# Kernel tuning notes

Hardware: AMD Instinct MI355X
Metric: run time of the kernel (lower is better)

Reference implementation:

```python
import jax, jax.numpy as jnp
import numpy as np

B, S, D, H = 2, 2048, 1024, 16
DH = D // H


def setup_inputs() -> dict:
    key = jax.random.key(0)
    ks = jax.random.split(key, 5)
    scale = 0.02
    return {
        "X": jax.random.normal(ks[0], (B, S, D), jnp.float32),
        "Wq": jax.random.normal(ks[1], (H, D, DH), jnp.float32) * scale,
        "Wk": jax.random.normal(ks[2], (H, D, DH), jnp.float32) * scale,
        "Wv": jax.random.normal(ks[3], (H, D, DH), jnp.float32) * scale,
        "Wo": jax.random.normal(ks[4], (D, D), jnp.float32) * scale,
        "bo": jnp.zeros((D,), jnp.float32),
    }


def reference(X, Wq, Wk, Wv, Wo, bo):
    # Per-head projections, batched over heads: [B,H,S,DH]
    Q = jnp.einsum('bsd,hde->bhse', X, Wq)
    K = jnp.einsum('bsd,hde->bhse', X, Wk)
    V = jnp.einsum('bsd,hde->bhse', X, Wv)
    # Scores scaled by sqrt(d_model) exactly as in the source (not sqrt(d_head))
    A = jnp.einsum('bhse,bhte->bhst', Q, K) / jnp.sqrt(jnp.float32(D))
    A = jax.nn.softmax(A, axis=-1)  # no mask in the source
    O = jnp.einsum('bhst,bhte->bhse', A, V)  # [B,H,S,DH]
    # Concat heads -> [B,S,D], then output projection
    O = jnp.transpose(O, (0, 2, 1, 3)).reshape(B, S, D)
    return O @ Wo + bo
```

## Files before the change

kernel.cpp:

```cpp
#include <hip/hip_runtime.h>
#include <math.h>

static constexpr int Bc  = 2;
static constexpr int Sc  = 2048;
static constexpr int Dc  = 1024;
static constexpr int Hc  = 16;
static constexpr int DHc = 64;

typedef short bf16x8 __attribute__((ext_vector_type(8)));
typedef float f32x4  __attribute__((ext_vector_type(4)));

static constexpr float LOG2E = 1.4426950408889634f;

static __device__ __forceinline__ unsigned short f2bf(float x) {
  union { float f; unsigned u; } v; v.f = x;
  unsigned r = v.u + 0x7FFFu + ((v.u >> 16) & 1u);
  return (unsigned short)(r >> 16);
}
static __device__ __forceinline__ float bf2f(unsigned short u) {
  union { unsigned u; float f; } v; v.u = ((unsigned)u) << 16;
  return v.f;
}
static __device__ __forceinline__ unsigned pk2bf_trunc(float a, float b) {
  return __builtin_amdgcn_perm(__float_as_uint(b), __float_as_uint(a), 0x07060302u);
}
#if __has_builtin(__builtin_amdgcn_exp2f)
#define EXP2F(x) __builtin_amdgcn_exp2f(x)
#else
#define EXP2F(x) exp2f(x)
#endif

static __device__ __forceinline__ void gload16(const void* g, void* l) {
  __builtin_amdgcn_global_load_lds(
      (const __attribute__((address_space(1))) void*)g,
      (__attribute__((address_space(3))) void*)l, 16, 0, 0);
}

__global__ __launch_bounds__(256) void prep(
    const float* __restrict__ Wq, const float* __restrict__ Wk,
    const float* __restrict__ Wv, const float* __restrict__ Wo,
    const float* __restrict__ X,
    unsigned short* __restrict__ Wt3, unsigned short* __restrict__ Wot,
    unsigned short* __restrict__ Xb) {
  const int z = blockIdx.z;
  if (z == 4) {
    size_t base = ((size_t)blockIdx.y * 16 + blockIdx.x) * 4096;
#pragma unroll
    for (int it = 0; it < 16; ++it) {
      size_t i = base + it * 256 + threadIdx.x;
      float4 v = ((const float4*)X)[i];
      ushort4 u; u.x = f2bf(v.x); u.y = f2bf(v.y); u.z = f2bf(v.z); u.w = f2bf(v.w);
      ((ushort4*)Xb)[i] = u;
    }
    return;
  }
  __shared__ unsigned short T[64][68];
  const float* src; unsigned short* dst;
  int srcld, dstld, r0, c0;
  if (z < 3) {
    const float* W = (z == 0) ? Wq : (z == 1) ? Wk : Wv;
    unsigned short* Wt = Wt3 + (size_t)z * Dc * Dc;
    int h = blockIdx.y;
    src = W + (size_t)h * Dc * DHc;  srcld = DHc; r0 = blockIdx.x * 64; c0 = 0;
    dst = Wt + (size_t)h * DHc * Dc; dstld = Dc;
  } else {
    src = Wo;  srcld = Dc; r0 = blockIdx.x * 64; c0 = blockIdx.y * 64;
    dst = Wot; dstld = Dc;
  }
#pragma unroll
  for (int it = 0; it < 16; ++it) {
    int idx = it * 256 + threadIdx.x;
    int r = idx >> 6, c = idx & 63;
    T[c][r] = f2bf(src[(size_t)(r0 + r) * srcld + c0 + c]);
  }
  __syncthreads();
#pragma unroll
  for (int it = 0; it < 4; ++it) {
    int idx = it * 256 + threadIdx.x;
    int c = idx >> 4, r4 = (idx & 15) * 4;
    ushort4 u = *(const ushort4*)&T[c][r4];
    *(ushort4*)&dst[(size_t)(c0 + c) * dstld + r0 + r4] = u;
  }
}

__global__ __launch_bounds__(512, 2) void qkv_gemm(
    const unsigned short* __restrict__ Xb, const unsigned short* __restrict__ Wt3,
    unsigned short* __restrict__ Qb, unsigned short* __restrict__ Kb,
    unsigned short* __restrict__ Vtb) {
  __shared__ alignas(16) unsigned char smem[135168];
  unsigned short (*S)[64] = (unsigned short(*)[64])smem;

  const int tid = threadIdx.x;
  const int wv = tid >> 6, lane = tid & 63;
  const int ln = lane & 15, qd = (lane >> 4) & 3;
  const int wm = wv >> 2, wn = wv & 3;
  const int lr = lane >> 3;
  const int gcol = ((lane & 7) ^ lr) * 8;
  const int paq = ln & 7;

  const int bid = blockIdx.x;
  const int l = (bid & 7) * 24 + (bid >> 3);
  const int xb = l & 15, y = l >> 4;
  const int m0 = xb * 256, n0 = y * 256;
  const int which = y >> 2;
  const int b = m0 >> 11, s0 = m0 & 2047;
  const int h0 = (y & 3) * 4;

  const unsigned short* Ap = Xb + (size_t)m0 * 1024;
  const unsigned short* Bp = Wt3 + (size_t)n0 * 1024;
  const int grow = wv * 16 + lr;

#define STG(gb, srow) do {                                                  \
    gload16((gb) + (size_t)grow * 1024 + gcol,       &S[(srow) + wv * 16][0]); \
    gload16((gb) + (size_t)(grow + 8) * 1024 + gcol, &S[(srow) + wv * 16 + 8][0]); \
  } while (0)

#define RD_A(mh, rowbase) do {                                              \
    _Pragma("unroll") for (int mt = 0; mt < 4; ++mt)                        \
      _Pragma("unroll") for (int ks = 0; ks < 2; ++ks)                      \
        af[mt][ks] = *(const bf16x8*)&S[(rowbase) + (mh) * 64 + mt * 16 + ln] \
                                       [((ks * 4 + qd) ^ paq) * 8];         \
  } while (0)

#define RD_B(nh, rowbase) do {                                              \
    _Pragma("unroll") for (int nt = 0; nt < 2; ++nt)                        \
      _Pragma("unroll") for (int ks = 0; ks < 2; ++ks)                      \
        bf[(nh) * 2 + nt][ks] = *(const bf16x8*)&S[(rowbase) + (nh) * 32 + nt * 16 + ln] \
                                                  [((ks * 4 + qd) ^ paq) * 8]; \
  } while (0)

#define MM(mh, nh) do {                                                     \
    _Pragma("unroll") for (int ks = 0; ks < 2; ++ks)                        \
      _Pragma("unroll") for (int mt = 0; mt < 4; ++mt)                      \
        _Pragma("unroll") for (int nt = 0; nt < 2; ++nt)                    \
          acc[(mh) * 4 + mt][(nh) * 2 + nt] =                               \
              __builtin_amdgcn_mfma_f32_16x16x32_bf16(                      \
                  af[mt][ks], bf[(nh) * 2 + nt][ks],                        \
                  acc[(mh) * 4 + mt][(nh) * 2 + nt], 0, 0, 0);              \
  } while (0)

#define BAR __builtin_amdgcn_s_barrier()
#define WAITL asm volatile("s_waitcnt lgkmcnt(0)" ::: "memory")
#define WAITV(n) asm volatile("s_waitcnt vmcnt(" #n ")" ::: "memory")
#define PRIO1 __builtin_amdgcn_s_setprio(1)
#define PRIO0 __builtin_amdgcn_s_setprio(0)

  f32x4 acc[8][4];
#pragma unroll
  for (int mt = 0; mt < 8; ++mt)
#pragma unroll
    for (int nt = 0; nt < 4; ++nt) acc[mt][nt] = (f32x4){0.f, 0.f, 0.f, 0.f};

  STG(Bp, 512);
  STG(Ap, 0);
  STG(Ap + 128 * 1024, 128);
  STG(Bp + 128 * 1024, 640);
  STG(Bp + 64, 768);
  STG(Ap + 64, 256);
  WAITV(4);
  BAR;

  bf16x8 af[4][2], bf[4][2];

  for (int j = 0; j < 8; ++j) {
    const int last = (j == 7);
    const unsigned short* Ak = Ap + j * 128;
    const unsigned short* Bk = Bp + j * 128;

    STG(Ak + 128 * 1024 + 64, 384);
    RD_A(0, wm * 128);
    RD_B(0, 512 + (wn >> 1) * 128 + (wn & 1) * 64);
    BAR; WAITL;
    PRIO1; MM(0, 0); PRIO0; BAR;
    STG(Bk + 128 * 1024 + 64, 896);
    RD_B(1, 512 + (wn >> 1) * 128 + (wn & 1) * 64);
    BAR; WAITL;
    PRIO1; MM(0, 1); PRIO0; BAR;
    if (!last) STG(Bk + 128, 512);
    RD_A(1, wm * 128);
    BAR; WAITL;
    PRIO1; MM(1, 0); PRIO0; BAR;
    if (!last) STG(Ak + 128, 0);
    BAR;
    PRIO1; MM(1, 1); PRIO0;
    if (last) { WAITV(0); } else { WAITV(4); }
    BAR;

    if (!last) STG(Ak + 128 * 1024 + 128, 128);
    RD_A(0, 256 + wm * 128);
    RD_B(0, 768 + (wn >> 1) * 128 + (wn & 1) * 64);
    BAR; WAITL;
    PRIO1; MM(0, 0); PRIO0; BAR;
    if (!last) STG(Bk + 128 * 1024 + 128, 640);
    RD_B(1, 768 + (wn >> 1) * 128 + (wn & 1) * 64);
    BAR; WAITL;
    PRIO1; MM(0, 1); PRIO0; BAR;
    if (!last) STG(Bk + 192, 768);
    RD_A(1, 256 + wm * 128);
    BAR; WAITL;
    PRIO1; MM(1, 0); PRIO0; BAR;
    if (!last) STG(Ak + 192, 256);
    BAR;
    PRIO1; MM(1, 1); PRIO0;
    if (!last) WAITV(4);
    BAR;
  }

  unsigned short* Ts = (unsigned short*)smem;
  if (which < 2) {
    unsigned short* Out = (which == 0) ? Qb : Kb;
    const float scale = (which == 0) ? (LOG2E / 32.0f) : 1.0f;
#pragma unroll
    for (int mt = 0; mt < 8; ++mt)
#pragma unroll
      for (int nt = 0; nt < 4; ++nt)
#pragma unroll
        for (int r = 0; r < 4; ++r)
          Ts[(wm * 128 + mt * 16 + qd * 4 + r) * 264 + wn * 64 + nt * 16 + ln] =
              f2bf(acc[mt][nt][r] * scale);
    __syncthreads();
    const int row = tid >> 1;
#pragma unroll
    for (int it = 0; it < 16; ++it) {
      int c16 = (tid & 1) * 16 + it;
      int head = c16 >> 3, e8 = c16 & 7;
      *(ulonglong2*)&Out[(((size_t)b * Hc + h0 + head) * Sc + s0 + row) * DHc + e8 * 8] =
          *(const ulonglong2*)&Ts[row * 264 + c16 * 8];
    }
  } else {
#pragma unroll
    for (int mt = 0; mt < 8; ++mt)
#pragma unroll
      for (int nt = 0; nt < 4; ++nt)
#pragma unroll
        for (int r = 0; r < 4; ++r)
          Ts[(wn * 64 + nt * 16 + ln) * 264 + wm * 128 + mt * 16 + qd * 4 + r] =
              f2bf(acc[mt][nt][r]);
    __syncthreads();
    const int n = tid >> 1;
    const int head = n >> 6, e = n & 63;
    unsigned short* dst = Vtb + (((size_t)b * Hc + h0 + head) * DHc + e) * Sc + s0;
#pragma unroll
    for (int it = 0; it < 16; ++it) {
      int s16 = (tid & 1) * 16 + it;
      *(ulonglong2*)&dst[s16 * 8] = *(const ulonglong2*)&Ts[n * 264 + s16 * 8];
    }
  }
#undef STG
#undef RD_A
#undef RD_B
#undef MM
#undef BAR
#undef WAITL
#undef WAITV
#undef PRIO1
#undef PRIO0
}

__global__ __launch_bounds__(256, 2) void attn_partial(
    const unsigned short* __restrict__ Qb, const unsigned short* __restrict__ Kb,
    const unsigned short* __restrict__ Vtb,
    unsigned short* __restrict__ Opart, float* __restrict__ lpart) {
  __shared__ alignas(16) unsigned short Ks[64][64];
  __shared__ alignas(16) unsigned short Vts[64][64];
  __shared__ alignas(16) unsigned short Ps[256][64];

  const int tid = threadIdx.x;
  const int wv = tid >> 6, lane = tid & 63;
  const int ln = tid & 15, qd = (tid >> 4) & 3;
  const int sT = blockIdx.x, bh = blockIdx.y, sp = blockIdx.z;
  const int lr = lane >> 3;
  const int lcs = ((lane & 7) ^ lr) * 8;

  bf16x8 qf[4][2];
  const size_t qrow0 = (size_t)bh * Sc + sT * 256 + wv * 64;
#pragma unroll
  for (int mt = 0; mt < 4; ++mt)
#pragma unroll
    for (int ks = 0; ks < 2; ++ks)
      qf[mt][ks] = *(const bf16x8*)&Qb[(qrow0 + mt * 16 + ln) * DHc + ks * 32 + qd * 8];

  bf16x8 vones;
#pragma unroll
  for (int j = 0; j < 8; ++j) vones[j] = (short)0x3F80;

  f32x4 o[4][4], lacc[4];
#pragma unroll
  for (int mt = 0; mt < 4; ++mt) {
    lacc[mt] = (f32x4){0.f, 0.f, 0.f, 0.f};
#pragma unroll
    for (int et = 0; et < 4; ++et) o[mt][et] = (f32x4){0.f, 0.f, 0.f, 0.f};
  }

  for (int kb = sp * 16; kb < sp * 16 + 16; ++kb) {
    __syncthreads();
#pragma unroll
    for (int t = 0; t < 2; ++t) {
      gload16(Kb  + ((size_t)bh * Sc + kb * 64 + wv * 16 + t * 8 + lr) * DHc + lcs,
              &Ks[wv * 16 + t * 8][0]);
      gload16(Vtb + ((size_t)bh * DHc + wv * 16 + t * 8 + lr) * Sc + kb * 64 + lcs,
              &Vts[wv * 16 + t * 8][0]);
    }
    __syncthreads();

    f32x4 st[4][4];
#pragma unroll
    for (int mt = 0; mt < 4; ++mt)
#pragma unroll
      for (int nt = 0; nt < 4; ++nt) st[mt][nt] = (f32x4){0.f, 0.f, 0.f, 0.f};
#pragma unroll
    for (int ks = 0; ks < 2; ++ks) {
      const int pa = ((ks * 4 + qd) ^ (ln & 7)) * 8;
#pragma unroll
      for (int nt = 0; nt < 4; ++nt) {
        bf16x8 kf = *(const bf16x8*)&Ks[nt * 16 + ln][pa];
#pragma unroll
        for (int mt = 0; mt < 4; ++mt)
          st[mt][nt] = __builtin_amdgcn_mfma_f32_16x16x32_bf16(kf, qf[mt][ks], st[mt][nt], 0, 0, 0);
      }
    }

#pragma unroll
    for (int mt = 0; mt < 4; ++mt) {
      const int prow = wv * 64 + mt * 16 + ln;
#pragma unroll
      for (int nt = 0; nt < 4; ++nt) {
        float p0 = EXP2F(st[mt][nt][0]);
        float p1 = EXP2F(st[mt][nt][1]);
        float p2 = EXP2F(st[mt][nt][2]);
        float p3 = EXP2F(st[mt][nt][3]);
        uint2 w;
        w.x = pk2bf_trunc(p0, p1);
        w.y = pk2bf_trunc(p2, p3);
        int ppos = ((2 * nt + (qd >> 1)) ^ (ln & 7)) * 8 + (qd & 1) * 4;
        *(uint2*)&Ps[prow][ppos] = w;
      }
    }
    __syncthreads();

#pragma unroll
    for (int ks = 0; ks < 2; ++ks) {
      const int pa = ((ks * 4 + qd) ^ (ln & 7)) * 8;
      bf16x8 pf[4];
#pragma unroll
      for (int mt = 0; mt < 4; ++mt) {
        pf[mt] = *(const bf16x8*)&Ps[wv * 64 + mt * 16 + ln][pa];
        lacc[mt] = __builtin_amdgcn_mfma_f32_16x16x32_bf16(pf[mt], vones, lacc[mt], 0, 0, 0);
      }
#pragma unroll
      for (int et = 0; et < 4; ++et) {
        bf16x8 vf = *(const bf16x8*)&Vts[et * 16 + ln][pa];
#pragma unroll
        for (int mt = 0; mt < 4; ++mt)
          o[mt][et] = __builtin_amdgcn_mfma_f32_16x16x32_bf16(pf[mt], vf, o[mt][et], 0, 0, 0);
      }
    }
  }

  const size_t pbase = (size_t)sp * 65536 + ((size_t)bh * 8 + sT) * 256;
  if (ln == 0) {
#pragma unroll
    for (int mt = 0; mt < 4; ++mt)
#pragma unroll
      for (int r = 0; r < 4; ++r)
        lpart[pbase + wv * 64 + mt * 16 + qd * 4 + r] = lacc[mt][r];
  }
#pragma unroll
  for (int mt = 0; mt < 4; ++mt)
#pragma unroll
    for (int r = 0; r < 4; ++r) {
      int row = wv * 64 + mt * 16 + qd * 4 + r;
#pragma unroll
      for (int et = 0; et < 4; ++et)
        Opart[(pbase + row) * DHc + et * 16 + ln] = f2bf(o[mt][et][r]);
    }
}

__global__ __launch_bounds__(256) void combine(
    const unsigned short* __restrict__ Opart, const float* __restrict__ lpart,
    unsigned short* __restrict__ Ocat) {
  const int sT = blockIdx.x, bh = blockIdx.y, tid = threadIdx.x;
  const int b = bh >> 4, h = bh & 15;
  const size_t p0 = ((size_t)bh * 8 + sT) * 256;
  const size_t p1 = p0 + 65536;
#pragma unroll
  for (int it = 0; it < 16; ++it) {
    int idx = it * 256 + tid;
    int row = idx >> 4, c4 = (idx & 15) * 4;
    ushort4 u0 = *(const ushort4*)&Opart[(p0 + row) * DHc + c4];
    ushort4 u1 = *(const ushort4*)&Opart[(p1 + row) * DHc + c4];
    float inv = 1.0f / (lpart[p0 + row] + lpart[p1 + row]);
    ushort4 w;
    w.x = f2bf((bf2f(u0.x) + bf2f(u1.x)) * inv);
    w.y = f2bf((bf2f(u0.y) + bf2f(u1.y)) * inv);
    w.z = f2bf((bf2f(u0.z) + bf2f(u1.z)) * inv);
    w.w = f2bf((bf2f(u0.w) + bf2f(u1.w)) * inv);
    *(ushort4*)&Ocat[((size_t)b * Sc + sT * 256 + row) * Dc + h * DHc + c4] = w;
  }
}

__global__ __launch_bounds__(256) void out_gemm(
    const unsigned short* __restrict__ Ab, const unsigned short* __restrict__ Wot,
    const float* __restrict__ bo, float* __restrict__ Out) {
  __shared__ alignas(16) unsigned short As[64][64];
  __shared__ alignas(16) unsigned short Bs[128][64];

  const int tid = threadIdx.x;
  const int wv = tid >> 6, lane = tid & 63;
  const int ln = tid & 15, qd = (tid >> 4) & 3;
  const int wm = wv >> 1, wn = wv & 1;
  const int m0 = blockIdx.x * 64, n0 = blockIdx.y * 128;
  const int lr = lane >> 3;
  const int lcs = ((lane & 7) ^ lr) * 8;

  f32x4 acc[2][4];
#pragma unroll
  for (int mt = 0; mt < 2; ++mt)
#pragma unroll
    for (int nt = 0; nt < 4; ++nt) acc[mt][nt] = (f32x4){0.f, 0.f, 0.f, 0.f};

  for (int k0 = 0; k0 < Dc; k0 += 64) {
    __syncthreads();
#pragma unroll
    for (int t = 0; t < 2; ++t)
      gload16(Ab + (size_t)(m0 + wv * 16 + t * 8 + lr) * Dc + k0 + lcs, &As[wv * 16 + t * 8][0]);
#pragma unroll
    for (int t = 0; t < 4; ++t)
      gload16(Wot + (size_t)(n0 + wv * 32 + t * 8 + lr) * Dc + k0 + lcs, &Bs[wv * 32 + t * 8][0]);
    __syncthreads();
#pragma unroll
    for (int ks = 0; ks < 2; ++ks) {
      const int pa = ((ks * 4 + qd) ^ (ln & 7)) * 8;
      bf16x8 af[2], bf[4];
#pragma unroll
      for (int mt = 0; mt < 2; ++mt)
        af[mt] = *(const bf16x8*)&As[wm * 32 + mt * 16 + ln][pa];
#pragma unroll
      for (int nt = 0; nt < 4; ++nt)
        bf[nt] = *(const bf16x8*)&Bs[wn * 64 + nt * 16 + ln][pa];
#pragma unroll
      for (int mt = 0; mt < 2; ++mt)
#pragma unroll
        for (int nt = 0; nt < 4; ++nt)
          acc[mt][nt] = __builtin_amdgcn_mfma_f32_16x16x32_bf16(af[mt], bf[nt], acc[mt][nt], 0, 0, 0);
    }
  }

  float bias[4];
#pragma unroll
  for (int nt = 0; nt < 4; ++nt) bias[nt] = bo[n0 + wn * 64 + nt * 16 + ln];

#pragma unroll
  for (int mt = 0; mt < 2; ++mt)
#pragma unroll
    for (int r = 0; r < 4; ++r) {
      int m = m0 + wm * 32 + mt * 16 + qd * 4 + r;
#pragma unroll
      for (int nt = 0; nt < 4; ++nt)
        Out[(size_t)m * Dc + n0 + wn * 64 + nt * 16 + ln] = acc[mt][nt][r] + bias[nt];
    }
}

extern "C" void kernel_launch(void* const* d_in, const int* in_sizes, int n_in,
                              void* d_out, int out_size, void* d_ws, size_t ws_size,
                              hipStream_t stream) {
  (void)in_sizes; (void)n_in; (void)out_size; (void)ws_size;
  const float* X  = (const float*)d_in[0];
  const float* Wq = (const float*)d_in[1];
  const float* Wk = (const float*)d_in[2];
  const float* Wv = (const float*)d_in[3];
  const float* Wo = (const float*)d_in[4];
  const float* bo = (const float*)d_in[5];
  float* out = (float*)d_out;

  const size_t nX = (size_t)Bc * Sc * Dc;
  unsigned short* Xb    = (unsigned short*)d_ws;
  unsigned short* Wt3   = Xb + nX;
  unsigned short* Wot   = Wt3 + (size_t)3 * Dc * Dc;
  unsigned short* Qb    = Wot + (size_t)Dc * Dc;
  unsigned short* Kb    = Qb + nX;
  unsigned short* Vtb   = Kb + nX;
  unsigned short* Opart = Vtb + nX;
  float* lpart = (float*)(Opart + 2 * nX);
  unsigned short* Ocat = Xb;

  prep<<<dim3(16, 16, 5), 256, 0, stream>>>(Wq, Wk, Wv, Wo, X, Wt3, Wot, Xb);
  qkv_gemm<<<dim3(192), 512, 0, stream>>>(Xb, Wt3, Qb, Kb, Vtb);
  attn_partial<<<dim3(8, 32, 2), 256, 0, stream>>>(Qb, Kb, Vtb, Opart, lpart);
  combine<<<dim3(8, 32), 256, 0, stream>>>(Opart, lpart, Ocat);
  out_gemm<<<dim3(64, 8), 256, 0, stream>>>(Ocat, Wot, bo, out);
}
```

Before: 183.9 us.

## Double-buffer K/V tiles in attention loop and remap block indices

The attention kernel now keeps two LDS buffers for the K and V tiles and prefetches the next tile while the current one is computed on. This is meant to hide global load latency behind the MFMA work. It also drops the barrier between writing and reading P, since each wave only touches its own rows, and raises wave priority around the MFMA groups. Block indices are permuted so neighbouring launched blocks map to a different mix of (tile, head, split), likely to improve cache locality across compute dies. In exchange, LDS use per block doubles for K and V, which could limit occupancy.

```diff
diff --git a/kernel.cpp b/kernel.cpp
--- a/kernel.cpp
+++ b/kernel.cpp
@@ -261,17 +261,24 @@
     const unsigned short* __restrict__ Qb, const unsigned short* __restrict__ Kb,
     const unsigned short* __restrict__ Vtb,
     unsigned short* __restrict__ Opart, float* __restrict__ lpart) {
-  __shared__ alignas(16) unsigned short Ks[64][64];
-  __shared__ alignas(16) unsigned short Vts[64][64];
+  __shared__ alignas(16) unsigned short Ks[2][64][64];
+  __shared__ alignas(16) unsigned short Vts[2][64][64];
   __shared__ alignas(16) unsigned short Ps[256][64];
 
   const int tid = threadIdx.x;
   const int wv = tid >> 6, lane = tid & 63;
   const int ln = tid & 15, qd = (tid >> 4) & 3;
-  const int sT = blockIdx.x, bh = blockIdx.y, sp = blockIdx.z;
+  const int l0 = blockIdx.x + 8 * blockIdx.y + 256 * blockIdx.z;
+  const int wid = (l0 & 7) * 64 + (l0 >> 3);
+  const int sT = wid & 7, bh = (wid >> 3) & 31, sp = wid >> 8;
   const int lr = lane >> 3;
   const int lcs = ((lane & 7) ^ lr) * 8;
 
+#define ABAR __builtin_amdgcn_s_barrier()
+#define AWAITV0 asm volatile("s_waitcnt vmcnt(0)" ::: "memory")
+#define APRIO1 __builtin_amdgcn_s_setprio(1)
+#define APRIO0 __builtin_amdgcn_s_setprio(0)
+
   bf16x8 qf[4][2];
   const size_t qrow0 = (size_t)bh * Sc + sT * 256 + wv * 64;
 #pragma unroll
@@ -292,16 +299,24 @@
     for (int et = 0; et < 4; ++et) o[mt][et] = (f32x4){0.f, 0.f, 0.f, 0.f};
   }
 
-  for (int kb = sp * 16; kb < sp * 16 + 16; ++kb) {
-    __syncthreads();
-#pragma unroll
-    for (int t = 0; t < 2; ++t) {
-      gload16(Kb  + ((size_t)bh * Sc + kb * 64 + wv * 16 + t * 8 + lr) * DHc + lcs,
-              &Ks[wv * 16 + t * 8][0]);
-      gload16(Vtb + ((size_t)bh * DHc + wv * 16 + t * 8 + lr) * Sc + kb * 64 + lcs,
-              &Vts[wv * 16 + t * 8][0]);
-    }
-    __syncthreads();
+#define ASTG(kb, buf) do {                                                   \
+    _Pragma("unroll") for (int t = 0; t < 2; ++t) {                          \
+      gload16(Kb + ((size_t)bh * Sc + (kb) * 64 + wv * 16 + t * 8 + lr) * DHc + lcs, \
+              &Ks[(buf)][wv * 16 + t * 8][0]);                               \
+      gload16(Vtb + ((size_t)bh * DHc + wv * 16 + t * 8 + lr) * Sc + (kb) * 64 + lcs, \
+              &Vts[(buf)][wv * 16 + t * 8][0]);                              \
+    }                                                                        \
+  } while (0)
+
+  ASTG(sp * 16, 0);
+  AWAITV0;
+  ABAR;
+
+#pragma unroll 2
+  for (int i = 0; i < 16; ++i) {
+    const int kb = sp * 16 + i;
+    const int cur = i & 1;
+    if (i < 15) ASTG(kb + 1, cur ^ 1);
 
     f32x4 st[4][4];
 #pragma unroll
@@ -313,10 +328,12 @@
       const int pa = ((ks * 4 + qd) ^ (ln & 7)) * 8;
 #pragma unroll
       for (int nt = 0; nt < 4; ++nt) {
-        bf16x8 kf = *(const bf16x8*)&Ks[nt * 16 + ln][pa];
+        bf16x8 kf = *(const bf16x8*)&Ks[cur][nt * 16 + ln][pa];
+        APRIO1;
 #pragma unroll
         for (int mt = 0; mt < 4; ++mt)
           st[mt][nt] = __builtin_amdgcn_mfma_f32_16x16x32_bf16(kf, qf[mt][ks], st[mt][nt], 0, 0, 0);
+        APRIO0;
       }
     }
 
@@ -336,7 +353,6 @@
         *(uint2*)&Ps[prow][ppos] = w;
       }
     }
-    __syncthreads();
 
 #pragma unroll
     for (int ks = 0; ks < 2; ++ks) {
@@ -349,12 +365,17 @@
       }
 #pragma unroll
       for (int et = 0; et < 4; ++et) {
-        bf16x8 vf = *(const bf16x8*)&Vts[et * 16 + ln][pa];
+        bf16x8 vf = *(const bf16x8*)&Vts[cur][et * 16 + ln][pa];
+        APRIO1;
 #pragma unroll
         for (int mt = 0; mt < 4; ++mt)
           o[mt][et] = __builtin_amdgcn_mfma_f32_16x16x32_bf16(pf[mt], vf, o[mt][et], 0, 0, 0);
+        APRIO0;
       }
     }
+
+    AWAITV0;
+    ABAR;
   }
 
   const size_t pbase = (size_t)sp * 65536 + ((size_t)bh * 8 + sT) * 256;
@@ -374,6 +395,11 @@
       for (int et = 0; et < 4; ++et)
         Opart[(pbase + row) * DHc + et * 16 + ln] = f2bf(o[mt][et][r]);
     }
+#undef ASTG
+#undef ABAR
+#undef AWAITV0
+#undef APRIO1
+#undef APRIO0
 }
 
 __global__ __launch_bounds__(256) void combine(
```

Measured after the change: 185.8 us. No clear change (+1.0%).
